# Kernel optimization log

Measured on AMD Instinct MI355X. Metric: run time of the kernel, lower is better.

The kernel has to match this reference:

```python
import jax, jax.numpy as jnp
import numpy as np

N = 200000   # active voxels
K = 27       # 3x3x3 kernel volume
CIN = 32
COUT = 64


def setup_inputs() -> dict:
    key = jax.random.key(0)
    k1, k2, k3, k4 = jax.random.split(key, 4)
    features = jax.random.normal(k1, (N, CIN), dtype=jnp.float32)
    # kernel map: for each kernel offset k and output voxel n, index of the
    # contributing input voxel (or masked out if that neighbor is inactive)
    neighbor_map = jax.random.randint(k2, (K, N), 0, N, dtype=jnp.int32)
    neighbor_mask = jax.random.randint(k3, (K, N), 0, 2) > 0
    std = 1.0 / float(np.sqrt(CIN * K))  # matches reset_parameters
    kernel = jax.random.uniform(k4, (K, CIN, COUT), dtype=jnp.float32,
                                minval=-std, maxval=std)
    return {"features": features, "neighbor_map": neighbor_map,
            "neighbor_mask": neighbor_mask, "kernel": kernel}


def reference(features, neighbor_map, neighbor_mask, kernel):
    # Sparse conv3d as gather -> per-offset matmul -> accumulate.
    # scan over the K=27 kernel offsets keeps peak memory at one gathered
    # [N, CIN] buffer instead of materializing [K, N, CIN].
    n_out = features.shape[0]
    cout = kernel.shape[-1]

    def body(acc, inp):
        nm_k, mask_k, w_k = inp  # [N], [N], [CIN, COUT]
        g = features[nm_k] * mask_k[:, None].astype(features.dtype)  # gather [N, CIN]
        return acc + g @ w_k, None

    init = jnp.zeros((n_out, cout), dtype=features.dtype)
    out, _ = jax.lax.scan(body, init, (neighbor_map, neighbor_mask, kernel))
    return out
```

## Files before the change

kernel.cpp:

```cpp
#include <hip/hip_runtime.h>

#define CIN   32
#define COUT  64
#define K_OFF 27

typedef __attribute__((ext_vector_type(8))) short bf16x8;
typedef __attribute__((ext_vector_type(4))) float f32x4;

#define FENCE_VM(N) asm volatile("s_waitcnt vmcnt(" #N ")" ::: "memory")
#define PIN()       asm volatile("" ::: "memory")
#define BARRIER()   asm volatile("s_barrier" ::: "memory")

__device__ inline unsigned short f2bf_rne(float f) {
    union { float f; unsigned int u; } v; v.f = f;
    unsigned int u = v.u;
    u = (u + 0x7fffu + ((u >> 16) & 1u)) >> 16;
    return (unsigned short)u;
}

__device__ inline void async_load16(const void* g, void* l) {
    __builtin_amdgcn_global_load_lds(
        (const __attribute__((address_space(1))) void*)g,
        (__attribute__((address_space(3))) void*)l, 16, 0, 0);
}

__global__ __launch_bounds__(256) void detect_mask(
    const unsigned char* __restrict__ mask, int nbytes, int* __restrict__ flag,
    float* __restrict__ zrow) {
    __shared__ int wany[4];
    int found = 0;
    for (int i = threadIdx.x; i < nbytes; i += 256)
        if ((i & 3) && mask[i]) found = 1;
    unsigned long long b = __ballot(found);
    if ((threadIdx.x & 63) == 0) wany[threadIdx.x >> 6] = b ? 1 : 0;
    __syncthreads();
    if (threadIdx.x == 0) *flag = wany[0] | wany[1] | wany[2] | wany[3];
    if (threadIdx.x < 16) zrow[threadIdx.x] = 0.0f;
}

__global__ __launch_bounds__(256) void prep_kernel(
    const float* __restrict__ feat, const int* __restrict__ nmap,
    const unsigned char* __restrict__ mask8, const int* __restrict__ mask32,
    const float* __restrict__ wk,
    unsigned short* __restrict__ featb, int* __restrict__ midx,
    unsigned short* __restrict__ wt2,
    int n, int Bf, int Bm, const int* __restrict__ flag)
{
    const int gid = blockIdx.x;
    if (gid < Bf) {
        const int base = (gid * 256 + threadIdx.x) * 8;
        if (base < n * CIN) {
            float4 a = *(const float4*)(feat + base);
            float4 b = *(const float4*)(feat + base + 4);
            bf16x8 v;
            v[0] = (short)f2bf_rne(a.x); v[1] = (short)f2bf_rne(a.y);
            v[2] = (short)f2bf_rne(a.z); v[3] = (short)f2bf_rne(a.w);
            v[4] = (short)f2bf_rne(b.x); v[5] = (short)f2bf_rne(b.y);
            v[6] = (short)f2bf_rne(b.z); v[7] = (short)f2bf_rne(b.w);
            *(bf16x8*)(featb + base) = v;
        }
    } else if (gid < Bf + Bm) {
        const int t = (gid - Bf) * 256 + threadIdx.x;
        int i = t * 4;
        const int total = K_OFF * n;
        const int is_b8 = *flag;
        if (i + 3 < total) {
            int4 nm = *(const int4*)(nmap + i);
            int m0, m1, m2, m3;
            if (is_b8) {
                uchar4 mb = *(const uchar4*)(mask8 + i);
                m0 = mb.x; m1 = mb.y; m2 = mb.z; m3 = mb.w;
            } else {
                int4 mm = *(const int4*)(mask32 + i);
                m0 = mm.x; m1 = mm.y; m2 = mm.z; m3 = mm.w;
            }
            int4 r;
            r.x = m0 ? nm.x : -1; r.y = m1 ? nm.y : -1;
            r.z = m2 ? nm.z : -1; r.w = m3 ? nm.w : -1;
            *(int4*)(midx + i) = r;
        } else {
            for (; i < total; ++i) {
                int m = is_b8 ? (int)mask8[i] : mask32[i];
                midx[i] = m ? nmap[i] : -1;
            }
        }
    } else {
        const int t = (gid - Bf - Bm) * 256 + threadIdx.x;
        if (t < K_OFF * 4 * 64) {
            const int lane = t & 63, ct = (t >> 6) & 3, k = t >> 8;
            const int lrow = lane & 15, q = lane >> 4;
            const int col = ct * 16 + lrow;
            bf16x8 v;
            #pragma unroll
            for (int j = 0; j < 8; ++j)
                v[j] = (short)f2bf_rne(wk[(k * CIN + q * 8 + j) * COUT + col]);
            *(bf16x8*)(wt2 + t * 8) = v;
        }
    }
}

__global__ __launch_bounds__(256) void conv_mfma10(
    const unsigned short* __restrict__ featb,
    const int*            __restrict__ midx,
    const unsigned short* __restrict__ wt2,
    const unsigned short* __restrict__ zrow,
    float* __restrict__ out, int n)
{
    __shared__ __attribute__((aligned(16))) unsigned short Bs[3][4][512];
    __shared__ __attribute__((aligned(16))) unsigned short As[3][4][2][512];

    const int tid  = threadIdx.x;
    const int wave = tid >> 6;
    const int lane = tid & 63;
    const int lrow = lane & 15;
    const int q    = lane >> 4;
    const int n0   = blockIdx.x * 128 + wave * 32;

    const int  row0 = n0 + lrow, row1 = n0 + 16 + lrow;
    const bool vr0 = row0 < n, vr1 = row1 < n;

    auto load_mi = [&](int k, int rt) -> int {
        const int  r = rt ? row1 : row0;
        const bool v = rt ? vr1 : vr0;
        if (!v) return -1;
        return midx[k * n + r];
    };
    auto issue_gather = [&](int mi, unsigned short* ldsbase) {
        const unsigned short* src =
            (mi >= 0) ? featb + (size_t)mi * CIN + q * 8 : zrow;
        async_load16(src, ldsbase);
    };
    auto stageB = [&](int k) {
        const unsigned short* src = wt2 + (((k * 4 + wave)) << 9) + lane * 8;
        async_load16(src, &Bs[k % 3][wave][0]);
    };

    int   mi_buf[2][2];
    f32x4 acc[2][4] = {};

    {
        int p00 = load_mi(0, 0), p01 = load_mi(0, 1);
        int p10 = load_mi(1, 0), p11 = load_mi(1, 1);
        mi_buf[0][0] = load_mi(2, 0); mi_buf[0][1] = load_mi(2, 1);
        mi_buf[1][0] = load_mi(3, 0); mi_buf[1][1] = load_mi(3, 1);
        PIN();
        stageB(0);
        stageB(1);
        PIN();
        issue_gather(p00, &As[0][wave][0][0]);
        issue_gather(p01, &As[0][wave][1][0]);
        PIN();
        issue_gather(p10, &As[1][wave][0][0]);
        issue_gather(p11, &As[1][wave][1][0]);
        PIN();
        FENCE_VM(2);
        BARRIER();
    }

    #pragma unroll
    for (int k = 0; k < K_OFF; ++k) {
        bf16x8 a0 = *(const bf16x8*)(&As[k % 3][wave][0][lane * 8]);
        bf16x8 a1 = *(const bf16x8*)(&As[k % 3][wave][1][lane * 8]);
        bf16x8 b0 = *(const bf16x8*)(&Bs[k % 3][0][lane * 8]);
        bf16x8 b1 = *(const bf16x8*)(&Bs[k % 3][1][lane * 8]);
        bf16x8 b2 = *(const bf16x8*)(&Bs[k % 3][2][lane * 8]);
        bf16x8 b3 = *(const bf16x8*)(&Bs[k % 3][3][lane * 8]);
        PIN();

        if (k + 2 < K_OFF) {
            stageB(k + 2);
            PIN();
            issue_gather(mi_buf[k & 1][0], &As[(k + 2) % 3][wave][0][0]);
            issue_gather(mi_buf[k & 1][1], &As[(k + 2) % 3][wave][1][0]);
            PIN();
        }
        if (k + 4 < K_OFF) {
            mi_buf[k & 1][0] = load_mi(k + 4, 0);
            mi_buf[k & 1][1] = load_mi(k + 4, 1);
            PIN();
        }

        acc[0][0] = __builtin_amdgcn_mfma_f32_16x16x32_bf16(a0, b0, acc[0][0], 0, 0, 0);
        acc[1][0] = __builtin_amdgcn_mfma_f32_16x16x32_bf16(a1, b0, acc[1][0], 0, 0, 0);
        acc[0][1] = __builtin_amdgcn_mfma_f32_16x16x32_bf16(a0, b1, acc[0][1], 0, 0, 0);
        acc[1][1] = __builtin_amdgcn_mfma_f32_16x16x32_bf16(a1, b1, acc[1][1], 0, 0, 0);
        acc[0][2] = __builtin_amdgcn_mfma_f32_16x16x32_bf16(a0, b2, acc[0][2], 0, 0, 0);
        acc[1][2] = __builtin_amdgcn_mfma_f32_16x16x32_bf16(a1, b2, acc[1][2], 0, 0, 0);
        acc[0][3] = __builtin_amdgcn_mfma_f32_16x16x32_bf16(a0, b3, acc[0][3], 0, 0, 0);
        acc[1][3] = __builtin_amdgcn_mfma_f32_16x16x32_bf16(a1, b3, acc[1][3], 0, 0, 0);

        if (k < K_OFF - 1) {
            if      (k == 0)  FENCE_VM(5);
            else if (k <= 22) FENCE_VM(7);
            else if (k == 23) FENCE_VM(5);
            else if (k == 24) FENCE_VM(3);
            else              FENCE_VM(0);
            BARRIER();
        }
    }

    #pragma unroll
    for (int rt = 0; rt < 2; ++rt)
        #pragma unroll
        for (int ct = 0; ct < 4; ++ct)
            #pragma unroll
            for (int r = 0; r < 4; ++r) {
                const int row = n0 + rt * 16 + q * 4 + r;
                if (row < n) out[(size_t)row * COUT + ct * 16 + lrow] = acc[rt][ct][r];
            }
}

#define BN 64
__global__ __launch_bounds__(256) void sparse_conv_fp32(
    const float* __restrict__ feat, const int* __restrict__ nmap,
    const unsigned char* __restrict__ mask8, const int* __restrict__ mask32,
    const float* __restrict__ wk, float* __restrict__ out,
    int n, const int* __restrict__ flag)
{
    __shared__ float A[CIN][BN];
    __shared__ float W[CIN][COUT];
    const int tid = threadIdx.x;
    const int n0 = blockIdx.x * BN;
    const int is_b8 = *flag;
    const int r0 = (tid >> 4) * 4, c0 = (tid & 15) * 4;
    const int grow = tid >> 2, gpart = tid & 3;
    float acc[4][4] = {};
    for (int k = 0; k < K_OFF; ++k) {
        {
            const int base = tid * 8;
            const float* wsrc = wk + (size_t)k * (CIN * COUT) + base;
            float4 w0 = ((const float4*)wsrc)[0];
            float4 w1 = ((const float4*)wsrc)[1];
            *(float4*)&W[base >> 6][base & 63] = w0;
            *(float4*)&W[base >> 6][(base & 63) + 4] = w1;
        }
        {
            const int gn = n0 + grow;
            float4 f0 = make_float4(0.f, 0.f, 0.f, 0.f), f1 = f0;
            if (gn < n) {
                const int idx = k * n + gn;
                const int m = is_b8 ? (int)mask8[idx] : mask32[idx];
                if (m) {
                    const float* fsrc = feat + (size_t)nmap[idx] * CIN + gpart * 8;
                    f0 = ((const float4*)fsrc)[0];
                    f1 = ((const float4*)fsrc)[1];
                }
            }
            const int cb = gpart * 8;
            A[cb+0][grow]=f0.x; A[cb+1][grow]=f0.y; A[cb+2][grow]=f0.z; A[cb+3][grow]=f0.w;
            A[cb+4][grow]=f1.x; A[cb+5][grow]=f1.y; A[cb+6][grow]=f1.z; A[cb+7][grow]=f1.w;
        }
        __syncthreads();
        #pragma unroll
        for (int c = 0; c < CIN; ++c) {
            const float4 a = *(const float4*)&A[c][r0];
            const float4 w = *(const float4*)&W[c][c0];
            acc[0][0]+=a.x*w.x; acc[0][1]+=a.x*w.y; acc[0][2]+=a.x*w.z; acc[0][3]+=a.x*w.w;
            acc[1][0]+=a.y*w.x; acc[1][1]+=a.y*w.y; acc[1][2]+=a.y*w.z; acc[1][3]+=a.y*w.w;
            acc[2][0]+=a.z*w.x; acc[2][1]+=a.z*w.y; acc[2][2]+=a.z*w.z; acc[2][3]+=a.z*w.w;
            acc[3][0]+=a.w*w.x; acc[3][1]+=a.w*w.y; acc[3][2]+=a.w*w.z; acc[3][3]+=a.w*w.w;
        }
        __syncthreads();
    }
    #pragma unroll
    for (int i = 0; i < 4; ++i) {
        const int orow = n0 + r0 + i;
        if (orow < n)
            *(float4*)&out[(size_t)orow * COUT + c0] =
                make_float4(acc[i][0], acc[i][1], acc[i][2], acc[i][3]);
    }
}

static inline size_t align16(size_t x) { return (x + 15) & ~(size_t)15; }

extern "C" void kernel_launch(void* const* d_in, const int* in_sizes, int n_in,
                              void* d_out, int out_size, void* d_ws, size_t ws_size,
                              hipStream_t stream) {
    const float*         feat = (const float*)d_in[0];
    const int*           nmap = (const int*)d_in[1];
    const unsigned char* m8   = (const unsigned char*)d_in[2];
    const int*           m32  = (const int*)d_in[2];
    const float*         wk   = (const float*)d_in[3];
    float*               out  = (float*)d_out;

    const int n = in_sizes[0] / CIN;
    int* flag = (int*)d_ws;
    float* zrow = (float*)((char*)d_ws + 64);

    const size_t feat_off   = 128;
    const size_t feat_bytes = (size_t)n * CIN * 2;
    const size_t midx_off   = align16(feat_off + feat_bytes);
    const size_t midx_bytes = (size_t)K_OFF * n * 4;
    const size_t wt2_off    = align16(midx_off + midx_bytes);
    const size_t wt2_bytes  = (size_t)K_OFF * 4 * 64 * 8 * 2;
    const size_t needed     = wt2_off + wt2_bytes;

    const int mask_elems = K_OFF * n;
    const int det_bytes  = mask_elems < 4096 ? mask_elems : 4096;
    detect_mask<<<1, 256, 0, stream>>>(m8, det_bytes, flag, zrow);

    if (ws_size >= needed) {
        unsigned short* featb = (unsigned short*)((char*)d_ws + feat_off);
        int*            midx  = (int*)((char*)d_ws + midx_off);
        unsigned short* wt2   = (unsigned short*)((char*)d_ws + wt2_off);
        const int Bf = (n * CIN / 8 + 255) / 256;
        const int Bm = ((K_OFF * n + 3) / 4 + 255) / 256;
        const int Bw = (K_OFF * 4 * 64 + 255) / 256;
        prep_kernel<<<Bf + Bm + Bw, 256, 0, stream>>>(
            feat, nmap, m8, m32, wk, featb, midx, wt2, n, Bf, Bm, flag);
        const int nblocks = (n + 127) / 128;
        conv_mfma10<<<nblocks, 256, 0, stream>>>(
            featb, midx, wt2, (const unsigned short*)zrow, out, n);
    } else {
        const int nb = (n + BN - 1) / BN;
        sparse_conv_fp32<<<nb, 256, 0, stream>>>(feat, nmap, m8, m32, wk, out, n, flag);
    }
}
```

Measured before the change: 167.4 us.

## Fuse mask application into conv kernel and drop midx prepass and detect launch

The separate pass that combined neighbor_map and mask into a masked index array (midx) is removed. The conv kernel now reads nmap and the mask directly, with one coalesced load per lane for 32 rows, and broadcasts the indices via shuffles. Mask-format detection moves into a spare block of the prep kernel, so the standalone detect launch goes away on the fast path. This removes a full read and write of a K*N int array and one kernel launch. In exchange the conv kernel's inner loop gains extra loads and shuffles, and it reads the flag that a concurrent block of the prep kernel writes, which is ordered only by the kernel boundary.

```diff
diff --git a/kernel.cpp b/kernel.cpp
--- a/kernel.cpp
+++ b/kernel.cpp
@@ -39,13 +39,13 @@
 }
 
 __global__ __launch_bounds__(256) void prep_kernel(
-    const float* __restrict__ feat, const int* __restrict__ nmap,
-    const unsigned char* __restrict__ mask8, const int* __restrict__ mask32,
+    const float* __restrict__ feat, const unsigned char* __restrict__ mask8,
     const float* __restrict__ wk,
-    unsigned short* __restrict__ featb, int* __restrict__ midx,
-    unsigned short* __restrict__ wt2,
-    int n, int Bf, int Bm, const int* __restrict__ flag)
+    unsigned short* __restrict__ featb, unsigned short* __restrict__ wt2,
+    int n, int Bf, int det_bytes, int* __restrict__ flag,
+    float* __restrict__ zrow)
 {
+    __shared__ int wany[4];
     const int gid = blockIdx.x;
     if (gid < Bf) {
         const int base = (gid * 256 + threadIdx.x) * 8;
@@ -59,33 +59,8 @@
             v[6] = (short)f2bf_rne(b.z); v[7] = (short)f2bf_rne(b.w);
             *(bf16x8*)(featb + base) = v;
         }
-    } else if (gid < Bf + Bm) {
+    } else if (gid < Bf + (K_OFF * 4 * 64) / 256) {
         const int t = (gid - Bf) * 256 + threadIdx.x;
-        int i = t * 4;
-        const int total = K_OFF * n;
-        const int is_b8 = *flag;
-        if (i + 3 < total) {
-            int4 nm = *(const int4*)(nmap + i);
-            int m0, m1, m2, m3;
-            if (is_b8) {
-                uchar4 mb = *(const uchar4*)(mask8 + i);
-                m0 = mb.x; m1 = mb.y; m2 = mb.z; m3 = mb.w;
-            } else {
-                int4 mm = *(const int4*)(mask32 + i);
-                m0 = mm.x; m1 = mm.y; m2 = mm.z; m3 = mm.w;
-            }
-            int4 r;
-            r.x = m0 ? nm.x : -1; r.y = m1 ? nm.y : -1;
-            r.z = m2 ? nm.z : -1; r.w = m3 ? nm.w : -1;
-            *(int4*)(midx + i) = r;
-        } else {
-            for (; i < total; ++i) {
-                int m = is_b8 ? (int)mask8[i] : mask32[i];
-                midx[i] = m ? nmap[i] : -1;
-            }
-        }
-    } else {
-        const int t = (gid - Bf - Bm) * 256 + threadIdx.x;
         if (t < K_OFF * 4 * 64) {
             const int lane = t & 63, ct = (t >> 6) & 3, k = t >> 8;
             const int lrow = lane & 15, q = lane >> 4;
@@ -96,15 +71,25 @@
                 v[j] = (short)f2bf_rne(wk[(k * CIN + q * 8 + j) * COUT + col]);
             *(bf16x8*)(wt2 + t * 8) = v;
         }
-    }
-}
-
-__global__ __launch_bounds__(256) void conv_mfma10(
+    } else {
+        int found = 0;
+        for (int i = threadIdx.x; i < det_bytes; i += 256)
+            if ((i & 3) && mask8[i]) found = 1;
+        unsigned long long b = __ballot(found);
+        if ((threadIdx.x & 63) == 0) wany[threadIdx.x >> 6] = b ? 1 : 0;
+        __syncthreads();
+        if (threadIdx.x == 0) *flag = wany[0] | wany[1] | wany[2] | wany[3];
+        if (threadIdx.x < 16) zrow[threadIdx.x] = 0.0f;
+    }
+}
+
+__global__ __launch_bounds__(256) void conv_mfma11(
     const unsigned short* __restrict__ featb,
-    const int*            __restrict__ midx,
+    const int*            __restrict__ nmap,
+    const unsigned char*  __restrict__ maskb,
     const unsigned short* __restrict__ wt2,
     const unsigned short* __restrict__ zrow,
-    float* __restrict__ out, int n)
+    float* __restrict__ out, int n, const int* __restrict__ flag)
 {
     __shared__ __attribute__((aligned(16))) unsigned short Bs[3][4][512];
     __shared__ __attribute__((aligned(16))) unsigned short As[3][4][2][512];
@@ -119,39 +104,50 @@
     const int  row0 = n0 + lrow, row1 = n0 + 16 + lrow;
     const bool vr0 = row0 < n, vr1 = row1 < n;
 
-    auto load_mi = [&](int k, int rt) -> int {
-        const int  r = rt ? row1 : row0;
-        const bool v = rt ? vr1 : vr0;
-        if (!v) return -1;
-        return midx[k * n + r];
+    const int  mshift = (*flag) ? 0 : 2;
+
+    const int  mrow = n0 + (lane & 31);
+    const bool rv   = mrow < n;
+    const int  ridx = rv ? mrow : (n - 1);
+
+    auto load_m = [&](int k, int& nm, int& mk) {
+        const size_t idx = (size_t)k * n + ridx;
+        nm = nmap[idx];
+        mk = (int)maskb[idx << mshift];
     };
     auto issue_gather = [&](int mi, unsigned short* ldsbase) {
         const unsigned short* src =
             (mi >= 0) ? featb + (size_t)mi * CIN + q * 8 : zrow;
         async_load16(src, ldsbase);
     };
+    auto issue_pair = [&](int nm, int mk, int s) {
+        const int mi32 = (rv && mk) ? nm : -1;
+        const int mi0  = __shfl(mi32, lrow);
+        const int mi1  = __shfl(mi32, lrow + 16);
+        issue_gather(mi0, &As[s][wave][0][0]);
+        issue_gather(mi1, &As[s][wave][1][0]);
+    };
     auto stageB = [&](int k) {
         const unsigned short* src = wt2 + (((k * 4 + wave)) << 9) + lane * 8;
         async_load16(src, &Bs[k % 3][wave][0]);
     };
 
-    int   mi_buf[2][2];
+    int   nm_buf[2], mk_buf[2];
     f32x4 acc[2][4] = {};
 
     {
-        int p00 = load_mi(0, 0), p01 = load_mi(0, 1);
-        int p10 = load_mi(1, 0), p11 = load_mi(1, 1);
-        mi_buf[0][0] = load_mi(2, 0); mi_buf[0][1] = load_mi(2, 1);
-        mi_buf[1][0] = load_mi(3, 0); mi_buf[1][1] = load_mi(3, 1);
+        int nm0, mk0, nm1, mk1;
+        load_m(0, nm0, mk0);
+        load_m(1, nm1, mk1);
+        load_m(2, nm_buf[0], mk_buf[0]);
+        load_m(3, nm_buf[1], mk_buf[1]);
         PIN();
         stageB(0);
         stageB(1);
         PIN();
-        issue_gather(p00, &As[0][wave][0][0]);
-        issue_gather(p01, &As[0][wave][1][0]);
-        PIN();
-        issue_gather(p10, &As[1][wave][0][0]);
-        issue_gather(p11, &As[1][wave][1][0]);
+        issue_pair(nm0, mk0, 0);
+        PIN();
+        issue_pair(nm1, mk1, 1);
         PIN();
         FENCE_VM(2);
         BARRIER();
@@ -170,13 +166,11 @@
         if (k + 2 < K_OFF) {
             stageB(k + 2);
             PIN();
-            issue_gather(mi_buf[k & 1][0], &As[(k + 2) % 3][wave][0][0]);
-            issue_gather(mi_buf[k & 1][1], &As[(k + 2) % 3][wave][1][0]);
+            issue_pair(nm_buf[k & 1], mk_buf[k & 1], (k + 2) % 3);
             PIN();
         }
         if (k + 4 < K_OFF) {
-            mi_buf[k & 1][0] = load_mi(k + 4, 0);
-            mi_buf[k & 1][1] = load_mi(k + 4, 1);
+            load_m(k + 4, nm_buf[k & 1], mk_buf[k & 1]);
             PIN();
         }
 
@@ -208,6 +202,7 @@
                 const int row = n0 + rt * 16 + q * 4 + r;
                 if (row < n) out[(size_t)row * COUT + ct * 16 + lrow] = acc[rt][ct][r];
             }
+    (void)vr0; (void)vr1;
 }
 
 #define BN 64
@@ -289,29 +284,25 @@
 
     const size_t feat_off   = 128;
     const size_t feat_bytes = (size_t)n * CIN * 2;
-    const size_t midx_off   = align16(feat_off + feat_bytes);
-    const size_t midx_bytes = (size_t)K_OFF * n * 4;
-    const size_t wt2_off    = align16(midx_off + midx_bytes);
+    const size_t wt2_off    = align16(feat_off + feat_bytes);
     const size_t wt2_bytes  = (size_t)K_OFF * 4 * 64 * 8 * 2;
     const size_t needed     = wt2_off + wt2_bytes;
 
     const int mask_elems = K_OFF * n;
     const int det_bytes  = mask_elems < 4096 ? mask_elems : 4096;
-    detect_mask<<<1, 256, 0, stream>>>(m8, det_bytes, flag, zrow);
 
     if (ws_size >= needed) {
         unsigned short* featb = (unsigned short*)((char*)d_ws + feat_off);
-        int*            midx  = (int*)((char*)d_ws + midx_off);
         unsigned short* wt2   = (unsigned short*)((char*)d_ws + wt2_off);
         const int Bf = (n * CIN / 8 + 255) / 256;
-        const int Bm = ((K_OFF * n + 3) / 4 + 255) / 256;
-        const int Bw = (K_OFF * 4 * 64 + 255) / 256;
-        prep_kernel<<<Bf + Bm + Bw, 256, 0, stream>>>(
-            feat, nmap, m8, m32, wk, featb, midx, wt2, n, Bf, Bm, flag);
+        const int Bw = (K_OFF * 4 * 64) / 256;
+        prep_kernel<<<Bf + Bw + 1, 256, 0, stream>>>(
+            feat, m8, wk, featb, wt2, n, Bf, det_bytes, flag, zrow);
         const int nblocks = (n + 127) / 128;
-        conv_mfma10<<<nblocks, 256, 0, stream>>>(
-            featb, midx, wt2, (const unsigned short*)zrow, out, n);
+        conv_mfma11<<<nblocks, 256, 0, stream>>>(
+            featb, nmap, m8, wt2, (const unsigned short*)zrow, out, n, flag);
     } else {
+        detect_mask<<<1, 256, 0, stream>>>(m8, det_bytes, flag, zrow);
         const int nb = (n + BN - 1) / BN;
         sparse_conv_fp32<<<nb, 256, 0, stream>>>(feat, nmap, m8, m32, wk, out, n, flag);
     }
```

Result: no change. 166.7 us (-0.4%).
